# Kernel optimization log

Measured on AMD Instinct MI355X. Metric: run time of the kernel, lower is better.

Reference implementation:

```python
import jax, jax.numpy as jnp
import numpy as np

B, T, M, C, H = 32, 128, 1290, 512, 8
NUM_BLOCKS = 4
MLP_LAYERS = 2
TOPK = 8


def _ln(x, g, b):
    mu = jnp.mean(x, -1, keepdims=True)
    var = jnp.mean((x - mu) ** 2, -1, keepdims=True)
    return (x - mu) / jnp.sqrt(var + 1e-5) * g + b


def setup_inputs() -> dict:
    key = jax.random.key(0)
    ks = jax.random.split(key, 12)

    def w(k, shape, s=0.02):
        return jax.random.normal(k, shape, jnp.float32) * s

    return {
        "ipts": jax.random.normal(ks[0], (B, T, C), jnp.float32),
        "memory": jax.random.normal(ks[1], (B, M, C), jnp.float32),
        "Wq": w(ks[2], (C, C)), "bq": jnp.zeros(C, jnp.float32),
        "Wk": w(ks[3], (C, C)), "bk": jnp.zeros(C, jnp.float32),
        "Wv": w(ks[4], (C, C)), "bv": jnp.zeros(C, jnp.float32),
        "Wm": w(ks[5], (C, C)), "bm": jnp.zeros(C, jnp.float32),  # shared attention_mlp layer
        "g1": jnp.ones(C, jnp.float32), "b1": jnp.zeros(C, jnp.float32),
        "g2": jnp.ones(C, jnp.float32), "b2": jnp.zeros(C, jnp.float32),
        "Wp": w(ks[6], (C, C)), "bp": jnp.zeros(C, jnp.float32),
        "rep_w": jax.random.normal(ks[7], (C,), jnp.float32),
        "Wig": w(ks[8], (C, 2 * C)), "big": jnp.zeros(2 * C, jnp.float32),
        "Wmg": w(ks[9], (C, 2 * C)), "bmg": jnp.zeros(2 * C, jnp.float32),
        "forget_bias": jnp.float32(1.0),
        "input_bias": jnp.float32(0.0),
    }


def reference(ipts, memory, Wq, bq, Wk, bk, Wv, bv, Wm, bm, g1, b1, g2, b2,
              Wp, bp, rep_w, Wig, big, Wmg, bmg, forget_bias, input_bias):
    Dh = C // H
    scale = 1.0 / np.sqrt(Dh)

    def heads(x):  # [B,L,C] -> [B,H,L,Dh]
        return x.reshape(x.shape[0], x.shape[1], H, Dh).transpose(0, 2, 1, 3)

    def mha(inp, mem, use_topk):
        # query from mem, key/value from inp (matches multi_head_attention(ipts, memory))
        q, k, v = heads(mem @ Wq + bq), heads(inp @ Wk + bk), heads(inp @ Wv + bv)
        att = jax.nn.softmax(jnp.einsum('bhqd,bhkd->bhqk', q, k) * scale, axis=-1)
        if use_topk:
            _, idx = jax.lax.top_k(att, TOPK)  # [B,H,Q,TOPK]
            mask = jnp.zeros_like(att)
            for i in range(TOPK):  # small fixed loop; avoids [.,.,.,K,L] blowup
                mask = mask + jax.nn.one_hot(idx[..., i], att.shape[-1], dtype=att.dtype)
            att = att * mask
        o = jnp.einsum('bhqk,bhkd->bhqd', att, v)
        return o.transpose(0, 2, 1, 3).reshape(o.shape[0], o.shape[2], C)

    inp = ipts @ Wp + bp  # input_projector, [B,T,C]
    mem = memory
    for _ in range(NUM_BLOCKS):
        mem = _ln(mem + mha(inp, mem, True), g1, b1)
        h = mem
        for _ in range(MLP_LAYERS):  # shared weights (ModuleList([lin]*L))
            h = jax.nn.relu(h @ Wm + bm)
        mem = _ln(mem + h, g2, b2)

    # gates (gate_style='unit')
    gi = jnp.mean(jax.nn.relu(rep_w * inp), axis=1) @ Wig + big  # [B,2C]
    gm = jnp.tanh(memory) @ Wmg + bmg                            # [B,M,2C]
    gates = gm + gi[:, None, :]
    ig = jax.nn.sigmoid(gates[..., :C] + input_bias)
    fg = jax.nn.sigmoid(gates[..., C:] + forget_bias)
    next_memory = ig * jnp.tanh(mem) + fg * memory

    # hx: query from inp, key/value from next_memory, no topk
    hx = mha(next_memory, inp, False)  # [B,T,C]
    return (next_memory, hx)
```

## Files before the change

### kernel.cpp

```cpp
#include <hip/hip_runtime.h>
#include <stdint.h>

typedef uint16_t u16;
typedef uint32_t u32;

#define DEVI __device__ __forceinline__

DEVI float b2f(u16 u) { return __uint_as_float(((u32)u) << 16); }
DEVI float blo(u32 u) { return __uint_as_float(u << 16); }
DEVI float bhi(u32 u) { return __uint_as_float(u & 0xffff0000u); }
DEVI u16 f2b(float f) {
  u32 x = __float_as_uint(f);
  return (u16)((x + 0x7fffu + ((x >> 16) & 1u)) >> 16);
}
DEVI u32 pack2(float a, float b) { return (u32)f2b(a) | ((u32)f2b(b) << 16); }
DEVI float sigm(float x) { return 1.f / (1.f + __expf(-x)); }
DEVI float ftanh(float x) { return 1.f - 2.f / (1.f + __expf(2.f * x)); }

typedef __bf16 bf16x8 __attribute__((ext_vector_type(8)));
typedef float f32x4 __attribute__((ext_vector_type(4)));

#define MFMA16(a, b, c) __builtin_amdgcn_mfma_f32_16x16x32_bf16(a, b, c, 0, 0, 0)

DEVI void gll16(const void* g, void* l) {
  __builtin_amdgcn_global_load_lds((const __attribute__((address_space(1))) void*)g,
                                   (__attribute__((address_space(3))) void*)l, 16, 0, 0);
}

DEVI u32 fmono(float s) {
  u32 x = __float_as_uint(s);
  return x ^ (((u32)((int)x >> 31)) | 0x80000000u);
}

DEVI void ced(u32& a, u32& b) {
  u32 hi = max(a, b), lo = min(a, b);
  a = hi; b = lo;
}
DEVI void sort8_desc(u32* v) {
  ced(v[0], v[1]); ced(v[2], v[3]); ced(v[4], v[5]); ced(v[6], v[7]);
  ced(v[0], v[2]); ced(v[1], v[3]); ced(v[4], v[6]); ced(v[5], v[7]);
  ced(v[1], v[2]); ced(v[5], v[6]);
  ced(v[0], v[4]); ced(v[1], v[5]); ced(v[2], v[6]); ced(v[3], v[7]);
  ced(v[2], v[4]); ced(v[3], v[5]);
  ced(v[1], v[2]); ced(v[3], v[4]); ced(v[5], v[6]);
}
DEVI void bitonic8_desc(u32* v) {
  ced(v[0], v[4]); ced(v[1], v[5]); ced(v[2], v[6]); ced(v[3], v[7]);
  ced(v[0], v[2]); ced(v[1], v[3]); ced(v[4], v[6]); ced(v[5], v[7]);
  ced(v[0], v[1]); ced(v[2], v[3]); ced(v[4], v[5]); ced(v[6], v[7]);
}
DEVI void merge_top8(u32* a, const u32* b) {
#pragma unroll
  for (int j = 0; j < 8; ++j) a[j] = max(a[j], b[7 - j]);
  bitonic8_desc(a);
}

__global__ void detect_kernel(const u16* __restrict__ x, int* __restrict__ flag) {
  if (threadIdx.x == 0 && blockIdx.x == 0) {
    int f = 0;
    for (int i = 0; i < 64; ++i) {
      u16 u = x[2 * i];
      int e = (u >> 7) & 0xFF;
      if (e > 131) f = 1;
    }
    *flag = f;
  }
}

struct CvtArgs {
  const void* src[23];
  int aoff[23];
  int n[23];
  int total;
};

__global__ __launch_bounds__(256) void convert_fused(CvtArgs a, u16* __restrict__ arena,
                                                     const int* __restrict__ flag) {
  int e4 = (blockIdx.x * 256 + threadIdx.x) * 4;
  if (e4 >= a.total) return;
  const char* sp = (const char*)a.src[0];
  int rel = e4, cnt = a.n[0];
#pragma unroll
  for (int j = 1; j < 23; ++j)
    if (e4 >= a.aoff[j]) { sp = (const char*)a.src[j]; rel = e4 - a.aoff[j]; cnt = a.n[j]; }
  const bool f32 = (*flag != 0);
  if (rel + 3 < cnt) {
    if (f32) {
      float4 v = *(const float4*)(sp + (size_t)rel * 4);
      uint2 o;
      o.x = pack2(v.x, v.y);
      o.y = pack2(v.z, v.w);
      *(uint2*)(arena + e4) = o;
    } else {
      *(uint2*)(arena + e4) = *(const uint2*)(sp + (size_t)rel * 2);
    }
  } else {
#pragma unroll
    for (int k = 0; k < 4; ++k) {
      u16 o = 0;
      if (rel + k < cnt)
        o = f32 ? f2b(((const float*)sp)[rel + k]) : ((const u16*)sp)[rel + k];
      arena[e4 + k] = o;
    }
  }
}

__global__ void biascat_kernel(const u16* __restrict__ bq, const u16* __restrict__ bk,
                               const u16* __restrict__ bv, u16* __restrict__ bqkv,
                               u16* __restrict__ bkv) {
  int t = threadIdx.x;
  bqkv[t] = bq[t];
  bqkv[512 + t] = bk[t];
  bqkv[1024 + t] = bv[t];
  bkv[t] = bk[t];
  bkv[512 + t] = bv[t];
}

template <int ACT>
__global__ __launch_bounds__(256, 4) void gemm_bt(
    const u16* __restrict__ A, const u16* __restrict__ Bt,
    const u16* __restrict__ bias, u16* __restrict__ Co, int Mtot, int Ntot, int nby) {
  __shared__ __align__(16) u16 smem[128 * 136];
  u16* aT = smem;
  u16* bT = smem + 128 * 64;
  const int tid = threadIdx.x;
  const int lane = tid & 63;
  const int w = tid >> 6;

  const int nwg = gridDim.x;
  const int orig = blockIdx.x;
  const int xcd = orig & 7, sq = orig >> 3;
  const int qd = nwg >> 3, rm = nwg & 7;
  const int wg = (xcd < rm ? xcd * (qd + 1) : rm * (qd + 1) + (xcd - rm) * qd) + sq;
  const int m0 = (wg / nby) * 128;
  const int n0 = (wg % nby) * 128;

  const int wm = (w & 1) << 6;
  const int wn = (w >> 1) << 6;

  f32x4 acc[4][4] = {};

  const u16* ga[4];
  const u16* gb[4];
#pragma unroll
  for (int q = 0; q < 4; ++q) {
    int j = q * 256 + tid;
    int r = j >> 3, s = j & 7;
    int c = (s ^ (r & 7)) * 8;
    int ra = m0 + r;
    if (ra >= Mtot) ra = Mtot - 1;
    ga[q] = A + (size_t)ra * 512 + c;
    gb[q] = Bt + (size_t)(n0 + r) * 512 + c;
  }

  for (int ko = 0; ko < 8; ++ko) {
    const int k0 = ko * 64;
#pragma unroll
    for (int q = 0; q < 4; ++q) {
      int j = q * 256 + tid;
      gll16(ga[q] + k0, aT + j * 8);
      gll16(gb[q] + k0, bT + j * 8);
    }
    __syncthreads();
#pragma unroll
    for (int ks = 0; ks < 2; ++ks) {
      bf16x8 af[4], bfr[4];
#pragma unroll
      for (int i = 0; i < 4; ++i) {
        int cch = ks * 4 + (lane >> 4);
        int r = wm + i * 16 + (lane & 15);
        af[i] = *(const bf16x8*)(aT + (r * 8 + (cch ^ (r & 7))) * 8);
        int rn = wn + i * 16 + (lane & 15);
        bfr[i] = *(const bf16x8*)(bT + (rn * 8 + (cch ^ (rn & 7))) * 8);
      }
#pragma unroll
      for (int i = 0; i < 4; ++i)
#pragma unroll
        for (int jn = 0; jn < 4; ++jn)
          acc[i][jn] = MFMA16(af[i], bfr[jn], acc[i][jn]);
    }
    __syncthreads();
  }

  u16* st = smem;
  const int cl = lane & 15;
  const int rg = lane >> 4;
#pragma unroll
  for (int jn = 0; jn < 4; ++jn) {
    int coll = wn + jn * 16 + cl;
    float bv = b2f(bias[n0 + coll]);
#pragma unroll
    for (int i = 0; i < 4; ++i) {
      int rowb = wm + i * 16 + rg * 4;
#pragma unroll
      for (int rr = 0; rr < 4; ++rr) {
        float vv = acc[i][jn][rr] + bv;
        if (ACT) vv = fmaxf(vv, 0.f);
        st[(rowb + rr) * 136 + coll] = f2b(vv);
      }
    }
  }
  __syncthreads();
#pragma unroll
  for (int t = 0; t < 8; ++t) {
    int idx = (t * 256 + tid) * 8;
    int r = idx >> 7;
    int c = idx & 127;
    int row = m0 + r;
    if (row < Mtot) {
      uint4 v = *(const uint4*)(st + r * 136 + c);
      *(uint4*)(Co + (size_t)row * Ntot + n0 + c) = v;
    }
  }
}

__global__ __launch_bounds__(256, 4) void gemm_gates(
    const u16* __restrict__ A, const u16* __restrict__ WmgTp,
    const u16* __restrict__ bmg, const u16* __restrict__ gi,
    const u16* __restrict__ memfin, const u16* __restrict__ mem_in,
    const u16* __restrict__ ibp, const u16* __restrict__ fbp,
    u16* __restrict__ nmbf, void* __restrict__ outp, const int* __restrict__ flag,
    int Mtot) {
  __shared__ __align__(16) u16 smem[128 * 136];
  u16* aT = smem;
  u16* bT = smem + 128 * 64;
  const int tid = threadIdx.x;
  const int lane = tid & 63;
  const int w = tid >> 6;

  const int nwg = gridDim.x;
  const int orig = blockIdx.x;
  const int xcd = orig & 7, sq = orig >> 3;
  const int qd = nwg >> 3, rm = nwg & 7;
  const int wg = (xcd < rm ? xcd * (qd + 1) : rm * (qd + 1) + (xcd - rm) * qd) + sq;
  const int m0 = (wg >> 3) * 128;
  const int n0h = (wg & 7) * 64;

  const int wm = (w & 1) << 6;
  const int wn = (w >> 1) << 6;

  f32x4 acc[4][4] = {};

  const u16* ga[4];
  const u16* gb[4];
#pragma unroll
  for (int q = 0; q < 4; ++q) {
    int j = q * 256 + tid;
    int r = j >> 3, s = j & 7;
    int c = (s ^ (r & 7)) * 8;
    int ra = m0 + r;
    if (ra >= Mtot) ra = Mtot - 1;
    ga[q] = A + (size_t)ra * 512 + c;
    int br = (r < 64) ? (n0h + r) : (512 + n0h + r - 64);
    gb[q] = WmgTp + (size_t)br * 512 + c;
  }

  for (int ko = 0; ko < 8; ++ko) {
    const int k0 = ko * 64;
#pragma unroll
    for (int q = 0; q < 4; ++q) {
      int j = q * 256 + tid;
      gll16(ga[q] + k0, aT + j * 8);
      gll16(gb[q] + k0, bT + j * 8);
    }
    __syncthreads();
#pragma unroll
    for (int ks = 0; ks < 2; ++ks) {
      bf16x8 af[4], bfr[4];
#pragma unroll
      for (int i = 0; i < 4; ++i) {
        int cch = ks * 4 + (lane >> 4);
        int r = wm + i * 16 + (lane & 15);
        af[i] = *(const bf16x8*)(aT + (r * 8 + (cch ^ (r & 7))) * 8);
        int rn = wn + i * 16 + (lane & 15);
        bfr[i] = *(const bf16x8*)(bT + (rn * 8 + (cch ^ (rn & 7))) * 8);
      }
#pragma unroll
      for (int i = 0; i < 4; ++i)
#pragma unroll
        for (int jn = 0; jn < 4; ++jn)
          acc[i][jn] = MFMA16(af[i], bfr[jn], acc[i][jn]);
    }
    __syncthreads();
  }

  u16* st = smem;
  const int cl = lane & 15;
  const int rg = lane >> 4;
#pragma unroll
  for (int jn = 0; jn < 4; ++jn) {
    int coll = wn + jn * 16 + cl;
    int bcol = (coll < 64) ? (n0h + coll) : (512 + n0h + coll - 64);
    float bv = b2f(bmg[bcol]);
#pragma unroll
    for (int i = 0; i < 4; ++i) {
      int rowb = wm + i * 16 + rg * 4;
#pragma unroll
      for (int rr = 0; rr < 4; ++rr)
        st[(rowb + rr) * 136 + coll] = f2b(acc[i][jn][rr] + bv);
    }
  }
  __syncthreads();

  const float ib = b2f(ibp[0]);
  const float fb = b2f(fbp[0]);
  const bool of32 = (*flag != 0);
#pragma unroll
  for (int t = 0; t < 4; ++t) {
    int chunk = t * 256 + tid;
    int rl = chunk >> 3;
    int c8 = (chunk & 7) * 8;
    int row = m0 + rl;
    if (row >= Mtot) continue;
    int b = row / 1290;
    size_t gidx = (size_t)row * 512 + n0h + c8;
    uint4 uig = *(const uint4*)(st + rl * 136 + c8);
    uint4 ufg = *(const uint4*)(st + rl * 136 + 64 + c8);
    uint4 ugi = *(const uint4*)(gi + b * 1024 + n0h + c8);
    uint4 ugf = *(const uint4*)(gi + b * 1024 + 512 + n0h + c8);
    uint4 umf = *(const uint4*)(memfin + gidx);
    uint4 umi = *(const uint4*)(mem_in + gidx);
    const u32* pig = (const u32*)&uig;
    const u32* pfg = (const u32*)&ufg;
    const u32* pgi = (const u32*)&ugi;
    const u32* pgf = (const u32*)&ugf;
    const u32* pmf = (const u32*)&umf;
    const u32* pmi = (const u32*)&umi;
    float v[8];
#pragma unroll
    for (int k = 0; k < 4; ++k) {
      float ig0 = sigm(blo(pig[k]) + blo(pgi[k]) + ib);
      float ig1 = sigm(bhi(pig[k]) + bhi(pgi[k]) + ib);
      float fg0 = sigm(blo(pfg[k]) + blo(pgf[k]) + fb);
      float fg1 = sigm(bhi(pfg[k]) + bhi(pgf[k]) + fb);
      v[2 * k] = ig0 * ftanh(blo(pmf[k])) + fg0 * blo(pmi[k]);
      v[2 * k + 1] = ig1 * ftanh(bhi(pmf[k])) + fg1 * bhi(pmi[k]);
    }
    uint4 o;
    u32* po = (u32*)&o;
#pragma unroll
    for (int k = 0; k < 4; ++k) po[k] = pack2(v[2 * k], v[2 * k + 1]);
    *(uint4*)(nmbf + gidx) = o;
    if (of32) {
      float4 f0, f1;
      f0.x = v[0]; f0.y = v[1]; f0.z = v[2]; f0.w = v[3];
      f1.x = v[4]; f1.y = v[5]; f1.z = v[6]; f1.w = v[7];
      *(float4*)((float*)outp + gidx) = f0;
      *(float4*)((float*)outp + gidx + 4) = f1;
    } else {
      *(uint4*)((u16*)outp + gidx) = o;
    }
  }
}

__global__ __launch_bounds__(256) void transpose_kernel(const u16* __restrict__ in,
                                                        u16* __restrict__ outb, int K, int N) {
  __shared__ u16 tile[32][33];
  const int tx = threadIdx.x & 31, ty = threadIdx.x >> 5;
  const int bx = blockIdx.x * 32;
  const int by = blockIdx.y * 32;
#pragma unroll
  for (int i = 0; i < 32; i += 8) tile[ty + i][tx] = in[(size_t)(by + ty + i) * N + bx + tx];
  __syncthreads();
#pragma unroll
  for (int i = 0; i < 32; i += 8) outb[(size_t)(bx + ty + i) * K + by + tx] = tile[tx][ty + i];
}

__global__ void tanhmem_kernel(const u16* __restrict__ mi, u16* __restrict__ th, int n8) {
  int i = blockIdx.x * 256 + threadIdx.x;
  if (i >= n8) return;
  uint4 u = ((const uint4*)mi)[i];
  uint4 t;
  t.x = pack2(ftanh(blo(u.x)), ftanh(bhi(u.x)));
  t.y = pack2(ftanh(blo(u.y)), ftanh(bhi(u.y)));
  t.z = pack2(ftanh(blo(u.z)), ftanh(bhi(u.z)));
  t.w = pack2(ftanh(blo(u.w)), ftanh(bhi(u.w)));
  ((uint4*)th)[i] = t;
}

__global__ void redmean_kernel(const u16* __restrict__ inp, const u16* __restrict__ repw,
                               u16* __restrict__ outb) {
  const int b = blockIdx.x;
  const int c = blockIdx.y * 256 + threadIdx.x;
  const float rw = b2f(repw[c]);
  float s = 0.f;
  for (int t = 0; t < 128; ++t)
    s += fmaxf(rw * b2f(inp[(size_t)(b * 128 + t) * 512 + c]), 0.f);
  outb[b * 512 + c] = f2b(s * (1.f / 128.f));
}

__global__ __launch_bounds__(64) void ln_kernel(const u16* __restrict__ src,
                                                const u16* __restrict__ addb,
                                                u16* __restrict__ dst,
                                                const u16* __restrict__ g,
                                                const u16* __restrict__ bb) {
  const int row = blockIdx.x;
  const int lane = threadIdx.x;
  const u16* srow = src + (size_t)row * 512;
  const u16* arow = addb + (size_t)row * 512;
  float x[8];
  float s = 0.f;
#pragma unroll
  for (int i = 0; i < 8; ++i) {
    int c = lane + i * 64;
    x[i] = b2f(srow[c]) + b2f(arow[c]);
    s += x[i];
  }
#pragma unroll
  for (int off = 32; off > 0; off >>= 1) s += __shfl_xor(s, off, 64);
  const float mu = s * (1.f / 512.f);
  float v = 0.f;
#pragma unroll
  for (int i = 0; i < 8; ++i) {
    float d = x[i] - mu;
    v = fmaf(d, d, v);
  }
#pragma unroll
  for (int off = 32; off > 0; off >>= 1) v += __shfl_xor(v, off, 64);
  const float rstd = rsqrtf(v * (1.f / 512.f) + 1e-5f);
  u16* orow = dst + (size_t)row * 512;
#pragma unroll
  for (int i = 0; i < 8; ++i) {
    int c = lane + i * 64;
    orow[c] = f2b(fmaf((x[i] - mu) * rstd, b2f(g[c]), b2f(bb[c])));
  }
}

__global__ __launch_bounds__(256, 3) void attn1_mfma(const u16* __restrict__ q,
                                                     const u16* __restrict__ kb,
                                                     const u16* __restrict__ vb,
                                                     u16* __restrict__ o, int ldkv) {
  __shared__ __align__(16) u16 Pl[128 * 136];
  __shared__ __align__(16) u16 VT[64 * 136];
  __shared__ float lbuf[128];
  u16* Kl = Pl;

  const int tid = threadIdx.x;
  const int lane = tid & 63;
  const int w = tid >> 6;
  const int quad = lane >> 4;
  const int l15 = lane & 15;
  const int qb = blockIdx.x;
  const int bh = blockIdx.y;
  const int b = bh >> 3, h = bh & 7;

#pragma unroll
  for (int qq = 0; qq < 4; ++qq) {
    int j = qq * 256 + tid;
    int r = j >> 3, s = j & 7;
    gll16(kb + (size_t)(b * 128 + r) * ldkv + h * 64 + (s ^ (r & 7)) * 8, Kl + j * 8);
  }
#pragma unroll
  for (int p = 0; p < 4; ++p) {
    int key = (tid & 63) + 64 * (p & 1);
    int dc = w + 4 * (p >> 1);
    uint4 u = *(const uint4*)(vb + (size_t)(b * 128 + key) * ldkv + h * 64 + dc * 8);
    u16 tmp[8];
    *(uint4*)tmp = u;
#pragma unroll
    for (int jj = 0; jj < 8; ++jj) VT[(dc * 8 + jj) * 136 + key] = tmp[jj];
  }

  bf16x8 bq[2][2];
  {
    int ra = min(qb * 128 + w * 32 + l15, 1289);
    int rb_ = min(qb * 128 + w * 32 + 16 + l15, 1289);
    const u16* qa = q + (size_t)(b * 1290 + ra) * 512 + h * 64 + quad * 8;
    const u16* qc = q + (size_t)(b * 1290 + rb_) * 512 + h * 64 + quad * 8;
    bq[0][0] = *(const bf16x8*)(qa);
    bq[0][1] = *(const bf16x8*)(qa + 32);
    bq[1][0] = *(const bf16x8*)(qc);
    bq[1][1] = *(const bf16x8*)(qc + 32);
  }
  __syncthreads();

  f32x4 sa[2][8] = {};
#pragma unroll
  for (int ks = 0; ks < 2; ++ks) {
#pragma unroll
    for (int jn = 0; jn < 8; ++jn) {
      int n = jn * 16 + l15;
      int cch = ks * 4 + quad;
      bf16x8 ak = *(const bf16x8*)(Kl + (n * 8 + (cch ^ (n & 7))) * 8);
      sa[0][jn] = MFMA16(ak, bq[0][ks], sa[0][jn]);
      sa[1][jn] = MFMA16(ak, bq[1][ks], sa[1][jn]);
    }
  }
  __syncthreads();

  const u32 ibase = 127u - (u32)(quad * 4);
#pragma unroll
  for (int i = 0; i < 2; ++i) {
    const int qi = w * 32 + i * 16 + l15;
    u32 g[4][8];
#pragma unroll
    for (int jn = 0; jn < 8; ++jn)
#pragma unroll
      for (int rr = 0; rr < 4; ++rr) {
        float s = sa[i][jn][rr] * 0.125f;
        sa[i][jn][rr] = s;
        g[jn >> 1][(jn & 1) * 4 + rr] =
            (fmono(s) & 0xFFFFFF80u) | (ibase - (u32)(jn * 16 + rr));
      }
    sort8_desc(g[0]); sort8_desc(g[1]); sort8_desc(g[2]); sort8_desc(g[3]);
    merge_top8(g[0], g[1]);
    merge_top8(g[2], g[3]);
    merge_top8(g[0], g[2]);
    u32* tv = g[0];
#pragma unroll
    for (int off = 16; off < 64; off <<= 1) {
      u32 pv[8];
#pragma unroll
      for (int j = 0; j < 8; ++j) pv[j] = (u32)__shfl_xor((int)tv[7 - j], off, 64);
#pragma unroll
      for (int j = 0; j < 8; ++j) tv[j] = max(tv[j], pv[j]);
      bitonic8_desc(tv);
    }
    const u32 t8 = tv[7];
    u32 mb = tv[0] & 0xFFFFFF80u;
    u32 xm = (mb & 0x80000000u) ? (mb ^ 0x80000000u) : ~mb;
    const float mx = __uint_as_float(xm);
    float lsum = 0.f;
#pragma unroll
    for (int jn = 0; jn < 8; ++jn) {
      u16 pr[4];
#pragma unroll
      for (int rr = 0; rr < 4; ++rr) {
        float s = sa[i][jn][rr];
        float e = __expf(s - mx);
        lsum += e;
        u32 kk = (fmono(s) & 0xFFFFFF80u) | (ibase - (u32)(jn * 16 + rr));
        pr[rr] = (kk >= t8) ? f2b(e) : (u16)0;
      }
      uint2 st;
      st.x = (u32)pr[0] | ((u32)pr[1] << 16);
      st.y = (u32)pr[2] | ((u32)pr[3] << 16);
      *(uint2*)(Pl + qi * 136 + jn * 16 + quad * 4) = st;
    }
    lsum += __shfl_xor(lsum, 16, 64);
    lsum += __shfl_xor(lsum, 32, 64);
    if (quad == 0) lbuf[qi] = 1.f / lsum;
  }
  __syncthreads();

  f32x4 oa[2][4] = {};
#pragma unroll
  for (int kc = 0; kc < 4; ++kc) {
    bf16x8 ap[2];
#pragma unroll
    for (int i = 0; i < 2; ++i)
      ap[i] = *(const bf16x8*)(Pl + (w * 32 + i * 16 + l15) * 136 + kc * 32 + quad * 8);
#pragma unroll
    for (int jd = 0; jd < 4; ++jd) {
      bf16x8 bv_ = *(const bf16x8*)(VT + (jd * 16 + l15) * 136 + kc * 32 + quad * 8);
      oa[0][jd] = MFMA16(ap[0], bv_, oa[0][jd]);
      oa[1][jd] = MFMA16(ap[1], bv_, oa[1][jd]);
    }
  }

#pragma unroll
  for (int i = 0; i < 2; ++i) {
    int rowl = w * 32 + i * 16 + quad * 4;
#pragma unroll
    for (int rr = 0; rr < 4; ++rr) {
      int qg = qb * 128 + rowl + rr;
      if (qg < 1290) {
        float il = lbuf[rowl + rr];
        u16* orow = o + (size_t)(b * 1290 + qg) * 512 + h * 64;
#pragma unroll
        for (int jd = 0; jd < 4; ++jd) orow[jd * 16 + l15] = f2b(oa[i][jd][rr] * il);
      }
    }
  }
}

__global__ __launch_bounds__(256, 2) void attn2_mfma(const u16* __restrict__ q2,
                                                     const u16* __restrict__ k2,
                                                     const u16* __restrict__ v2,
                                                     float* __restrict__ pacc,
                                                     float* __restrict__ pml,
                                                     int ldq, int ldkv) {
  __shared__ __align__(16) u16 Kl[64 * 64];
  __shared__ __align__(16) u16 VT[64 * 72];
  __shared__ __align__(16) u16 Pl[4 * 32 * 72];
  const int tid = threadIdx.x;
  const int lane = tid & 63;
  const int w = tid >> 6;
  const int quad = lane >> 4;
  const int l15 = lane & 15;
  const int bh = blockIdx.x;
  const int b = bh >> 3, h = bh & 7;
  const int part = blockIdx.y;
  const int kstart = (part * 1290) >> 2;
  const int kend = ((part + 1) * 1290) >> 2;

  bf16x8 aq[2][2];
  {
    int r0 = b * 128 + w * 32 + l15;
    const u16* qa = q2 + (size_t)r0 * ldq + h * 64 + quad * 8;
    aq[0][0] = *(const bf16x8*)(qa);
    aq[0][1] = *(const bf16x8*)(qa + 32);
    aq[1][0] = *(const bf16x8*)(qa + (size_t)16 * ldq);
    aq[1][1] = *(const bf16x8*)(qa + (size_t)16 * ldq + 32);
  }

  f32x4 oa[2][4] = {};
  float m_[2][4], l_[2][4];
#pragma unroll
  for (int i = 0; i < 2; ++i)
#pragma unroll
    for (int r = 0; r < 4; ++r) { m_[i][r] = -1e30f; l_[i][r] = 0.f; }

  const int nk = kend - kstart;
  for (int kt = 0; kt < nk; kt += 64) {
    __syncthreads();
#pragma unroll
    for (int qq = 0; qq < 2; ++qq) {
      int j = qq * 256 + tid;
      int r = j >> 3, s = j & 7;
      int kg = kstart + kt + r;
      if (kg >= kend) kg = kend - 1;
      gll16(k2 + (size_t)(b * 1290 + kg) * ldkv + h * 64 + (s ^ (r & 7)) * 8, Kl + j * 8);
    }
    {
      int r = tid & 63;
      int kg = kstart + kt + r;
      if (kg >= kend) kg = kend - 1;
      const u16* vrow = v2 + (size_t)(b * 1290 + kg) * ldkv + h * 64;
#pragma unroll
      for (int p = 0; p < 2; ++p) {
        int dc = (tid >> 6) + p * 4;
        uint4 u = *(const uint4*)(vrow + dc * 8);
        u16 tmp[8];
        *(uint4*)tmp = u;
#pragma unroll
        for (int jj = 0; jj < 8; ++jj) VT[(dc * 8 + jj) * 72 + r] = tmp[jj];
      }
    }
    __syncthreads();

    f32x4 sa[2][4] = {};
#pragma unroll
    for (int ks = 0; ks < 2; ++ks) {
#pragma unroll
      for (int jn = 0; jn < 4; ++jn) {
        int n = jn * 16 + l15;
        int cch = ks * 4 + quad;
        bf16x8 bk = *(const bf16x8*)(Kl + (n * 8 + (cch ^ (n & 7))) * 8);
        sa[0][jn] = MFMA16(aq[0][ks], bk, sa[0][jn]);
        sa[1][jn] = MFMA16(aq[1][ks], bk, sa[1][jn]);
      }
    }

    u16* pw = Pl + w * (32 * 72);
#pragma unroll
    for (int i = 0; i < 2; ++i) {
      float rmax[4] = {-1e30f, -1e30f, -1e30f, -1e30f};
#pragma unroll
      for (int jn = 0; jn < 4; ++jn) {
        int kg = kstart + kt + jn * 16 + l15;
        bool val = kg < kend;
#pragma unroll
        for (int r = 0; r < 4; ++r) {
          float s = sa[i][jn][r] * 0.125f;
          s = val ? s : -1e30f;
          sa[i][jn][r] = s;
          rmax[r] = fmaxf(rmax[r], s);
        }
      }
#pragma unroll
      for (int off = 1; off < 16; off <<= 1)
#pragma unroll
        for (int r = 0; r < 4; ++r) rmax[r] = fmaxf(rmax[r], __shfl_xor(rmax[r], off, 64));
      float alpha[4];
#pragma unroll
      for (int r = 0; r < 4; ++r) {
        float mn = fmaxf(m_[i][r], rmax[r]);
        alpha[r] = __expf(m_[i][r] - mn);
        m_[i][r] = mn;
      }
      float lsum[4] = {0.f, 0.f, 0.f, 0.f};
#pragma unroll
      for (int jn = 0; jn < 4; ++jn)
#pragma unroll
        for (int r = 0; r < 4; ++r) {
          float p = __expf(sa[i][jn][r] - m_[i][r]);
          sa[i][jn][r] = p;
          lsum[r] += p;
        }
#pragma unroll
      for (int off = 1; off < 16; off <<= 1)
#pragma unroll
        for (int r = 0; r < 4; ++r) lsum[r] += __shfl_xor(lsum[r], off, 64);
#pragma unroll
      for (int r = 0; r < 4; ++r) l_[i][r] = l_[i][r] * alpha[r] + lsum[r];
#pragma unroll
      for (int jd = 0; jd < 4; ++jd)
#pragma unroll
        for (int r = 0; r < 4; ++r) oa[i][jd][r] *= alpha[r];
#pragma unroll
      for (int jn = 0; jn < 4; ++jn) {
        int col = jn * 16 + l15;
#pragma unroll
        for (int r = 0; r < 4; ++r)
          pw[(i * 16 + quad * 4 + r) * 72 + col] = f2b(sa[i][jn][r]);
      }
    }

#pragma unroll
    for (int ks = 0; ks < 2; ++ks) {
      bf16x8 ap[2];
#pragma unroll
      for (int i = 0; i < 2; ++i)
        ap[i] = *(const bf16x8*)(pw + (i * 16 + l15) * 72 + ks * 32 + quad * 8);
#pragma unroll
      for (int jd = 0; jd < 4; ++jd) {
        bf16x8 bv_ = *(const bf16x8*)(VT + (jd * 16 + l15) * 72 + ks * 32 + quad * 8);
        oa[0][jd] = MFMA16(ap[0], bv_, oa[0][jd]);
        oa[1][jd] = MFMA16(ap[1], bv_, oa[1][jd]);
      }
    }
  }

  float* pa = pacc + (size_t)(part * 256 + bh) * 128 * 64;
#pragma unroll
  for (int i = 0; i < 2; ++i) {
    int row = w * 32 + i * 16 + quad * 4;
#pragma unroll
    for (int r = 0; r < 4; ++r)
#pragma unroll
      for (int jd = 0; jd < 4; ++jd)
        pa[(size_t)(row + r) * 64 + jd * 16 + l15] = oa[i][jd][r];
    if (l15 == 0) {
#pragma unroll
      for (int r = 0; r < 4; ++r) {
        size_t pi = (size_t)(part * 256 + bh) * 128 + row + r;
        pml[pi * 2 + 0] = m_[i][r];
        pml[pi * 2 + 1] = l_[i][r];
      }
    }
  }
}

__global__ __launch_bounds__(64) void attn2_merge(const float* __restrict__ pacc,
                                                  const float* __restrict__ pml,
                                                  void* __restrict__ outp,
                                                  const int* __restrict__ flag) {
  const int qi = blockIdx.x;
  const int bh = qi >> 7, t = qi & 127;
  const int b = bh >> 3, h = bh & 7;
  const int lane = threadIdx.x;
  float mv[4], lv[4];
  float m0 = -1e30f;
#pragma unroll
  for (int i = 0; i < 4; ++i) {
    size_t pi = (size_t)(i * 256 + bh) * 128 + t;
    mv[i] = pml[pi * 2];
    lv[i] = pml[pi * 2 + 1];
    m0 = fmaxf(m0, mv[i]);
  }
  float L = 0.f, accd = 0.f;
#pragma unroll
  for (int i = 0; i < 4; ++i) {
    size_t pi = (size_t)(i * 256 + bh) * 128 + t;
    float e = __expf(mv[i] - m0);
    L += lv[i] * e;
    accd += pacc[pi * 64 + lane] * e;
  }
  float v = accd / L;
  size_t off = (size_t)41280 * 512 + ((size_t)(b * 128 + t) * 512 + h * 64 + lane);
  if (*flag) ((float*)outp)[off] = v; else ((u16*)outp)[off] = f2b(v);
}

extern "C" void kernel_launch(void* const* d_in, const int* in_sizes, int n_in,
                              void* d_out, int out_size, void* d_ws, size_t ws_size,
                              hipStream_t stream) {
  (void)out_size; (void)ws_size;
  char* ws = (char*)d_ws;
  size_t off = 0;
  auto alloc = [&](size_t bytes) {
    char* p = ws + off;
    off += (bytes + 255) & ~(size_t)255;
    return (void*)p;
  };

  int* flag = (int*)alloc(256);

  size_t aoffs[32];
  size_t total = 0;
  for (int i = 0; i < n_in; ++i) {
    aoffs[i] = total;
    total += ((size_t)in_sizes[i] + 127) & ~(size_t)127;
  }
  u16* arena = (u16*)alloc(total * 2);

  const u16* c_ipts = arena + aoffs[0];
  const u16* c_mem  = arena + aoffs[1];
  const u16* c_Wq = arena + aoffs[2];  const u16* c_bq = arena + aoffs[3];
  const u16* c_Wk = arena + aoffs[4];  const u16* c_bk = arena + aoffs[5];
  const u16* c_Wv = arena + aoffs[6];  const u16* c_bv = arena + aoffs[7];
  const u16* c_Wm = arena + aoffs[8];  const u16* c_bm = arena + aoffs[9];
  const u16* c_g1 = arena + aoffs[10]; const u16* c_b1 = arena + aoffs[11];
  const u16* c_g2 = arena + aoffs[12]; const u16* c_b2 = arena + aoffs[13];
  const u16* c_Wp = arena + aoffs[14]; const u16* c_bp = arena + aoffs[15];
  const u16* c_repw = arena + aoffs[16];
  const u16* c_Wig = arena + aoffs[17]; const u16* c_big = arena + aoffs[18];
  const u16* c_Wmg = arena + aoffs[19]; const u16* c_bmg = arena + aoffs[20];
  const u16* c_fb = arena + aoffs[21];
  const u16* c_ib = arena + aoffs[22];

  u16* WqkvT = (u16*)alloc((size_t)1536 * 512 * 2);
  u16* WmT = (u16*)alloc(512 * 512 * 2);
  u16* WpT = (u16*)alloc(512 * 512 * 2);
  u16* WigT = (u16*)alloc(512 * 1024 * 2);
  u16* WmgT = (u16*)alloc(512 * 1024 * 2);
  u16* bqkv = (u16*)alloc(1536 * 2);
  u16* bkv = (u16*)alloc(1024 * 2);
  u16* inp = (u16*)alloc((size_t)4096 * 512 * 2);
  u16* qkvbuf = (u16*)alloc((size_t)4096 * 1536 * 2);
  u16* rmean = (u16*)alloc(32 * 512 * 2);
  u16* gi = (u16*)alloc(32 * 1024 * 2);
  u16* membf = (u16*)alloc((size_t)41280 * 512 * 2);
  u16* qbuf = (u16*)alloc((size_t)41280 * 512 * 2);
  u16* obuf = (u16*)alloc((size_t)41280 * 512 * 2);
  u16* gmbuf = (u16*)alloc((size_t)41280 * 512 * 2);
  u16* nmbf = (u16*)alloc((size_t)41280 * 512 * 2);
  (void)gmbuf;
  u16* kvbuf = obuf;
  float* pacc = (float*)(void*)qbuf;
  float* pml = (float*)((char*)(void*)qbuf + (size_t)4 * 32768 * 64 * 4);

  detect_kernel<<<1, 64, 0, stream>>>((const u16*)d_in[0], flag);
  {
    CvtArgs ca;
    for (int i = 0; i < 23; ++i) {
      int ii = (i < n_in) ? i : (n_in - 1);
      ca.src[i] = d_in[ii];
      ca.aoff[i] = (int)aoffs[ii];
      ca.n[i] = in_sizes[ii];
    }
    ca.total = (int)total;
    convert_fused<<<(unsigned)((total / 4 + 255) / 256), 256, 0, stream>>>(ca, arena, flag);
  }
  biascat_kernel<<<1, 512, 0, stream>>>(c_bq, c_bk, c_bv, bqkv, bkv);

  transpose_kernel<<<dim3(16, 16), 256, 0, stream>>>(c_Wq, WqkvT, 512, 512);
  transpose_kernel<<<dim3(16, 16), 256, 0, stream>>>(c_Wk, WqkvT + (size_t)512 * 512, 512, 512);
  transpose_kernel<<<dim3(16, 16), 256, 0, stream>>>(c_Wv, WqkvT + (size_t)1024 * 512, 512, 512);
  transpose_kernel<<<dim3(16, 16), 256, 0, stream>>>(c_Wm, WmT, 512, 512);
  transpose_kernel<<<dim3(16, 16), 256, 0, stream>>>(c_Wp, WpT, 512, 512);
  transpose_kernel<<<dim3(32, 16), 256, 0, stream>>>(c_Wig, WigT, 512, 1024);
  transpose_kernel<<<dim3(32, 16), 256, 0, stream>>>(c_Wmg, WmgT, 512, 1024);

  gemm_bt<0><<<dim3(32 * 4), 256, 0, stream>>>(c_ipts, WpT, c_bp, inp, 4096, 512, 4);
  gemm_bt<0><<<dim3(32 * 12), 256, 0, stream>>>(inp, WqkvT, bqkv, qkvbuf, 4096, 1536, 12);

  redmean_kernel<<<dim3(32, 2), 256, 0, stream>>>(inp, c_repw, rmean);
  gemm_bt<0><<<dim3(1 * 8), 256, 0, stream>>>(rmean, WigT, c_big, gi, 32, 1024, 8);

  const u16* memsrc = c_mem;
  for (int it = 0; it < 4; ++it) {
    gemm_bt<0><<<dim3(323 * 4), 256, 0, stream>>>(memsrc, WqkvT, c_bq, qbuf, 41280, 512, 4);
    attn1_mfma<<<dim3(11, 256), 256, 0, stream>>>(qbuf, qkvbuf + 512, qkvbuf + 1024, obuf, 1536);
    ln_kernel<<<dim3(41280), 64, 0, stream>>>(memsrc, obuf, membf, c_g1, c_b1);
    gemm_bt<1><<<dim3(323 * 4), 256, 0, stream>>>(membf, WmT, c_bm, qbuf, 41280, 512, 4);
    gemm_bt<1><<<dim3(323 * 4), 256, 0, stream>>>(qbuf, WmT, c_bm, obuf, 41280, 512, 4);
    ln_kernel<<<dim3(41280), 64, 0, stream>>>(membf, obuf, membf, c_g2, c_b2);
    memsrc = membf;
  }

  tanhmem_kernel<<<dim3(2641920 / 256), 256, 0, stream>>>(c_mem, qbuf, 2641920);
  gemm_gates<<<dim3(323 * 8), 256, 0, stream>>>(qbuf, WmgT, c_bmg, gi, membf, c_mem,
                                                c_ib, c_fb, nmbf, d_out, flag, 41280);

  gemm_bt<0><<<dim3(323 * 8), 256, 0, stream>>>(nmbf, WqkvT + (size_t)512 * 512, bkv,
                                                kvbuf, 41280, 1024, 8);
  attn2_mfma<<<dim3(256, 4), 256, 0, stream>>>(qkvbuf, kvbuf, kvbuf + 512, pacc, pml,
                                               1536, 1024);
  attn2_merge<<<dim3(32768), 64, 0, stream>>>(pacc, pml, d_out, flag);
}
```

Measured before the change: 1.246 ms.

## Double-buffer GEMM K-tiles in LDS and pack four LayerNorm rows per block

The two MFMA GEMM kernels now split K into 32-wide tiles held in two LDS buffers. The next tile's global-to-LDS load is issued before computing on the current one, with one barrier per step instead of two, so loads can overlap compute. The LDS swizzle is reworked for the 4-chunk rows. Separately, the LayerNorm kernel runs four rows per 256-thread block instead of one row per 64-thread block, cutting block count and scheduling overhead. The shorter K step halves the MFMA work between barriers and doubles the loop iterations.

```diff
diff --git a/kernel.cpp b/kernel.cpp
--- a/kernel.cpp
+++ b/kernel.cpp
@@ -121,11 +121,15 @@
     const u16* __restrict__ A, const u16* __restrict__ Bt,
     const u16* __restrict__ bias, u16* __restrict__ Co, int Mtot, int Ntot, int nby) {
   __shared__ __align__(16) u16 smem[128 * 136];
-  u16* aT = smem;
-  u16* bT = smem + 128 * 64;
+  u16* const aB0 = smem;
+  u16* const aB1 = smem + 4096;
+  u16* const bB0 = smem + 8192;
+  u16* const bB1 = smem + 12288;
   const int tid = threadIdx.x;
   const int lane = tid & 63;
   const int w = tid >> 6;
+  const int quad = lane >> 4;
+  const int l15 = lane & 15;
 
   const int nwg = gridDim.x;
   const int orig = blockIdx.x;
@@ -140,51 +144,57 @@
 
   f32x4 acc[4][4] = {};
 
-  const u16* ga[4];
-  const u16* gb[4];
-#pragma unroll
-  for (int q = 0; q < 4; ++q) {
+  const u16* ga[2];
+  const u16* gb[2];
+#pragma unroll
+  for (int q = 0; q < 2; ++q) {
     int j = q * 256 + tid;
-    int r = j >> 3, s = j & 7;
-    int c = (s ^ (r & 7)) * 8;
+    int r = j >> 2, s = j & 3;
+    int c = (s ^ ((r >> 1) & 3)) * 8;
     int ra = m0 + r;
     if (ra >= Mtot) ra = Mtot - 1;
     ga[q] = A + (size_t)ra * 512 + c;
     gb[q] = Bt + (size_t)(n0 + r) * 512 + c;
   }
 
-  for (int ko = 0; ko < 8; ++ko) {
-    const int k0 = ko * 64;
-#pragma unroll
-    for (int q = 0; q < 4; ++q) {
+  auto stage = [&](int p, int ko) {
+    u16* ab = p ? aB1 : aB0;
+    u16* bb = p ? bB1 : bB0;
+#pragma unroll
+    for (int q = 0; q < 2; ++q) {
       int j = q * 256 + tid;
-      gll16(ga[q] + k0, aT + j * 8);
-      gll16(gb[q] + k0, bT + j * 8);
-    }
+      gll16(ga[q] + ko * 32, ab + j * 8);
+      gll16(gb[q] + ko * 32, bb + j * 8);
+    }
+  };
+
+  stage(0, 0);
+  __syncthreads();
+  int cur = 0;
+  for (int ko = 0; ko < 16; ++ko) {
+    if (ko < 15) stage(cur ^ 1, ko + 1);
+    u16* ab = cur ? aB1 : aB0;
+    u16* bb = cur ? bB1 : bB0;
+    bf16x8 af[4], bfr[4];
+#pragma unroll
+    for (int i = 0; i < 4; ++i) {
+      int r = wm + i * 16 + l15;
+      af[i] = *(const bf16x8*)(ab + (((r << 2) | (quad ^ ((r >> 1) & 3)))) * 8);
+      int rn = wn + i * 16 + l15;
+      bfr[i] = *(const bf16x8*)(bb + (((rn << 2) | (quad ^ ((rn >> 1) & 3)))) * 8);
+    }
+#pragma unroll
+    for (int i = 0; i < 4; ++i)
+#pragma unroll
+      for (int jn = 0; jn < 4; ++jn)
+        acc[i][jn] = MFMA16(af[i], bfr[jn], acc[i][jn]);
     __syncthreads();
-#pragma unroll
-    for (int ks = 0; ks < 2; ++ks) {
-      bf16x8 af[4], bfr[4];
-#pragma unroll
-      for (int i = 0; i < 4; ++i) {
-        int cch = ks * 4 + (lane >> 4);
-        int r = wm + i * 16 + (lane & 15);
-        af[i] = *(const bf16x8*)(aT + (r * 8 + (cch ^ (r & 7))) * 8);
-        int rn = wn + i * 16 + (lane & 15);
-        bfr[i] = *(const bf16x8*)(bT + (rn * 8 + (cch ^ (rn & 7))) * 8);
-      }
-#pragma unroll
-      for (int i = 0; i < 4; ++i)
-#pragma unroll
-        for (int jn = 0; jn < 4; ++jn)
-          acc[i][jn] = MFMA16(af[i], bfr[jn], acc[i][jn]);
-    }
-    __syncthreads();
+    cur ^= 1;
   }
 
   u16* st = smem;
-  const int cl = lane & 15;
-  const int rg = lane >> 4;
+  const int cl = l15;
+  const int rg = quad;
 #pragma unroll
   for (int jn = 0; jn < 4; ++jn) {
     int coll = wn + jn * 16 + cl;
@@ -222,11 +232,15 @@
     u16* __restrict__ nmbf, void* __restrict__ outp, const int* __restrict__ flag,
     int Mtot) {
   __shared__ __align__(16) u16 smem[128 * 136];
-  u16* aT = smem;
-  u16* bT = smem + 128 * 64;
+  u16* const aB0 = smem;
+  u16* const aB1 = smem + 4096;
+  u16* const bB0 = smem + 8192;
+  u16* const bB1 = smem + 12288;
   const int tid = threadIdx.x;
   const int lane = tid & 63;
   const int w = tid >> 6;
+  const int quad = lane >> 4;
+  const int l15 = lane & 15;
 
   const int nwg = gridDim.x;
   const int orig = blockIdx.x;
@@ -241,13 +255,13 @@
 
   f32x4 acc[4][4] = {};
 
-  const u16* ga[4];
-  const u16* gb[4];
-#pragma unroll
-  for (int q = 0; q < 4; ++q) {
+  const u16* ga[2];
+  const u16* gb[2];
+#pragma unroll
+  for (int q = 0; q < 2; ++q) {
     int j = q * 256 + tid;
-    int r = j >> 3, s = j & 7;
-    int c = (s ^ (r & 7)) * 8;
+    int r = j >> 2, s = j & 3;
+    int c = (s ^ ((r >> 1) & 3)) * 8;
     int ra = m0 + r;
     if (ra >= Mtot) ra = Mtot - 1;
     ga[q] = A + (size_t)ra * 512 + c;
@@ -255,46 +269,50 @@
     gb[q] = WmgTp + (size_t)br * 512 + c;
   }
 
-  for (int ko = 0; ko < 8; ++ko) {
-    const int k0 = ko * 64;
-#pragma unroll
-    for (int q = 0; q < 4; ++q) {
+  auto stage = [&](int p, int ko) {
+    u16* ab = p ? aB1 : aB0;
+    u16* bb = p ? bB1 : bB0;
+#pragma unroll
+    for (int q = 0; q < 2; ++q) {
       int j = q * 256 + tid;
-      gll16(ga[q] + k0, aT + j * 8);
-      gll16(gb[q] + k0, bT + j * 8);
-    }
+      gll16(ga[q] + ko * 32, ab + j * 8);
+      gll16(gb[q] + ko * 32, bb + j * 8);
+    }
+  };
+
+  stage(0, 0);
+  __syncthreads();
+  int cur = 0;
+  for (int ko = 0; ko < 16; ++ko) {
+    if (ko < 15) stage(cur ^ 1, ko + 1);
+    u16* ab = cur ? aB1 : aB0;
+    u16* bb = cur ? bB1 : bB0;
+    bf16x8 af[4], bfr[4];
+#pragma unroll
+    for (int i = 0; i < 4; ++i) {
+      int r = wm + i * 16 + l15;
+      af[i] = *(const bf16x8*)(ab + (((r << 2) | (quad ^ ((r >> 1) & 3)))) * 8);
+      int rn = wn + i * 16 + l15;
+      bfr[i] = *(const bf16x8*)(bb + (((rn << 2) | (quad ^ ((rn >> 1) & 3)))) * 8);
+    }
+#pragma unroll
+    for (int i = 0; i < 4; ++i)
+#pragma unroll
+      for (int jn = 0; jn < 4; ++jn)
+        acc[i][jn] = MFMA16(af[i], bfr[jn], acc[i][jn]);
     __syncthreads();
-#pragma unroll
-    for (int ks = 0; ks < 2; ++ks) {
-      bf16x8 af[4], bfr[4];
-#pragma unroll
-      for (int i = 0; i < 4; ++i) {
-        int cch = ks * 4 + (lane >> 4);
-        int r = wm + i * 16 + (lane & 15);
-        af[i] = *(const bf16x8*)(aT + (r * 8 + (cch ^ (r & 7))) * 8);
-        int rn = wn + i * 16 + (lane & 15);
-        bfr[i] = *(const bf16x8*)(bT + (rn * 8 + (cch ^ (rn & 7))) * 8);
-      }
-#pragma unroll
-      for (int i = 0; i < 4; ++i)
-#pragma unroll
-        for (int jn = 0; jn < 4; ++jn)
-          acc[i][jn] = MFMA16(af[i], bfr[jn], acc[i][jn]);
-    }
-    __syncthreads();
+    cur ^= 1;
   }
 
   u16* st = smem;
-  const int cl = lane & 15;
-  const int rg = lane >> 4;
 #pragma unroll
   for (int jn = 0; jn < 4; ++jn) {
-    int coll = wn + jn * 16 + cl;
+    int coll = wn + jn * 16 + l15;
     int bcol = (coll < 64) ? (n0h + coll) : (512 + n0h + coll - 64);
     float bv = b2f(bmg[bcol]);
 #pragma unroll
     for (int i = 0; i < 4; ++i) {
-      int rowb = wm + i * 16 + rg * 4;
+      int rowb = wm + i * 16 + quad * 4;
 #pragma unroll
       for (int rr = 0; rr < 4; ++rr)
         st[(rowb + rr) * 136 + coll] = f2b(acc[i][jn][rr] + bv);
@@ -389,13 +407,13 @@
   outb[b * 512 + c] = f2b(s * (1.f / 128.f));
 }
 
-__global__ __launch_bounds__(64) void ln_kernel(const u16* __restrict__ src,
-                                                const u16* __restrict__ addb,
-                                                u16* __restrict__ dst,
-                                                const u16* __restrict__ g,
-                                                const u16* __restrict__ bb) {
-  const int row = blockIdx.x;
-  const int lane = threadIdx.x;
+__global__ __launch_bounds__(256) void ln_kernel(const u16* __restrict__ src,
+                                                 const u16* __restrict__ addb,
+                                                 u16* __restrict__ dst,
+                                                 const u16* __restrict__ g,
+                                                 const u16* __restrict__ bb) {
+  const int row = blockIdx.x * 4 + (threadIdx.x >> 6);
+  const int lane = threadIdx.x & 63;
   const u16* srow = src + (size_t)row * 512;
   const u16* arow = addb + (size_t)row * 512;
   float x[8];
@@ -862,10 +880,10 @@
   for (int it = 0; it < 4; ++it) {
     gemm_bt<0><<<dim3(323 * 4), 256, 0, stream>>>(memsrc, WqkvT, c_bq, qbuf, 41280, 512, 4);
     attn1_mfma<<<dim3(11, 256), 256, 0, stream>>>(qbuf, qkvbuf + 512, qkvbuf + 1024, obuf, 1536);
-    ln_kernel<<<dim3(41280), 64, 0, stream>>>(memsrc, obuf, membf, c_g1, c_b1);
+    ln_kernel<<<dim3(10320), 256, 0, stream>>>(memsrc, obuf, membf, c_g1, c_b1);
     gemm_bt<1><<<dim3(323 * 4), 256, 0, stream>>>(membf, WmT, c_bm, qbuf, 41280, 512, 4);
     gemm_bt<1><<<dim3(323 * 4), 256, 0, stream>>>(qbuf, WmT, c_bm, obuf, 41280, 512, 4);
-    ln_kernel<<<dim3(41280), 64, 0, stream>>>(membf, obuf, membf, c_g2, c_b2);
+    ln_kernel<<<dim3(10320), 256, 0, stream>>>(membf, obuf, membf, c_g2, c_b2);
     memsrc = membf;
   }
 
```

Measured after the change: 1.188 ms. -4.6%, faster.
